# Kernel tuning notes

Measured on AMD Instinct MI355X. Metric: run time of the kernel, lower is better.

## Reference

```python
import jax, jax.numpy as jnp
import numpy as np

DIM = 64
HID = DIM // 8  # 8, hidden width of pos_fc / attn_fc
B, N, V = 1024, 64, 8
NUM_IDS = 10


def setup_inputs() -> dict:
    key = jax.random.key(0)
    ks = jax.random.split(key, 24)
    stdv = 1.0 / np.sqrt(DIM * DIM)
    inp = {
        "q": jax.random.normal(ks[0], (B, N, DIM), jnp.float32),
        "k": jax.random.normal(ks[1], (B, N, V, DIM), jnp.float32),
        "pos": jax.random.normal(ks[2], (B, N, V, 4), jnp.float32),
        "strength": jax.random.normal(ks[3], (512,), jnp.float32),
        # learned params
        "q_tbl": jax.random.uniform(ks[4], (NUM_IDS, DIM * DIM), jnp.float32, -stdv, stdv),
        "k_tbl": jax.random.uniform(ks[5], (NUM_IDS, DIM * DIM), jnp.float32, -stdv, stdv),
        "v_tbl": jax.random.uniform(ks[6], (NUM_IDS, DIM * DIM), jnp.float32, -stdv, stdv),
        "pos_w1": jax.random.normal(ks[7], (4, HID), jnp.float32) * 0.5,
        "pos_b1": jax.random.normal(ks[8], (HID,), jnp.float32) * 0.1,
        "pos_w2": jax.random.normal(ks[9], (HID, DIM), jnp.float32) * 0.2,
        "pos_b2": jax.random.normal(ks[10], (DIM,), jnp.float32) * 0.1,
        "attn_w1": jax.random.normal(ks[11], (DIM, HID), jnp.float32) * 0.1,
        "attn_b1": jax.random.normal(ks[12], (HID,), jnp.float32) * 0.1,
        "attn_w2": jax.random.normal(ks[13], (HID, DIM), jnp.float32) * 0.2,
        "attn_b2": jax.random.normal(ks[14], (DIM,), jnp.float32) * 0.1,
        "out_w": jax.random.normal(ks[15], (DIM, DIM), jnp.float32) * 0.1,
        "out_b": jax.random.normal(ks[16], (DIM,), jnp.float32) * 0.1,
        "str_w": jax.random.normal(ks[17], (512, DIM), jnp.float32) * 0.04,
        "str_b": jax.random.normal(ks[18], (DIM,), jnp.float32) * 0.1,
        # int args
        "mask": jax.random.randint(ks[19], (B, N, V, 1), 0, 2, jnp.int32),
        "embed_id1": 3,
    }
    return inp


def reference(q, k, pos, strength, q_tbl, k_tbl, v_tbl,
              pos_w1, pos_b1, pos_w2, pos_b2,
              attn_w1, attn_b1, attn_w2, attn_b2,
              out_w, out_b, str_w, str_b, mask, embed_id1):
    s = strength @ str_w + str_b                       # [DIM]
    Wq = q_tbl[embed_id1].reshape(DIM, DIM)
    Wk = k_tbl[embed_id1].reshape(DIM, DIM)
    Wv = v_tbl[embed_id1].reshape(DIM, DIM)
    # F.linear(x, W) = x @ W.T ; note v is computed from k (as in source)
    qh = q @ Wq.T + s                                  # [B,N,DIM]
    kh = k @ Wk.T + s                                  # [B,N,V,DIM]
    vh = k @ Wv.T + s                                  # [B,N,V,DIM]
    p = jax.nn.relu(pos @ pos_w1 + pos_b1) @ pos_w2 + pos_b2   # [B,N,V,DIM]
    attn = kh - qh[:, :, None, :] + p                  # [B,N,V,DIM]
    attn = jax.nn.relu(attn @ attn_w1 + attn_b1) @ attn_w2 + attn_b2
    attn = jnp.where(mask == 0, jnp.float32(-1e9), attn)
    attn = jax.nn.softmax(attn, axis=-2)               # softmax over views V
    x = ((vh + p) * attn).sum(axis=2)                  # [B,N,DIM]
    x = x @ out_w + out_b
    return x
```

## Files before the change

### kernel.cpp

```cpp
#include <hip/hip_runtime.h>

#define TBL 4096

#define WS_S    0
#define WS_AT   64
#define WS_BQT  (64 + 512)
#define WS_CT   (64 + 1024)
#define WS_C0   (64 + 1024 + 64)

typedef __attribute__((ext_vector_type(8))) short bf16x8;
typedef __attribute__((ext_vector_type(4))) float f32x4;

__device__ inline short f2bf(float f) {
    union { float f; unsigned u; } v; v.f = f;
    unsigned r = v.u + 0x7fffu + ((v.u >> 16) & 1u);
    return (short)(r >> 16);
}

__device__ inline bf16x8 pack8(const float* x) {
    bf16x8 r;
    #pragma unroll
    for (int i = 0; i < 8; ++i) r[i] = f2bf(x[i]);
    return r;
}

__device__ inline bf16x8 loadpack(const float* p) {
    float4 a = *(const float4*)p;
    float4 b = *(const float4*)(p + 4);
    float t[8] = {a.x, a.y, a.z, a.w, b.x, b.y, b.z, b.w};
    return pack8(t);
}

__device__ inline bf16x8 loadpackneg(const float* p) {
    float4 a = *(const float4*)p;
    float4 b = *(const float4*)(p + 4);
    float t[8] = {-a.x, -a.y, -a.z, -a.w, -b.x, -b.y, -b.z, -b.w};
    return pack8(t);
}

__global__ __launch_bounds__(256) void precompute_kernel(
    const float* __restrict__ strength, const float* __restrict__ str_w,
    const float* __restrict__ str_b,
    const float* __restrict__ q_tbl, const float* __restrict__ k_tbl,
    const float* __restrict__ attn_w1, const float* __restrict__ attn_b1,
    const float* __restrict__ pos_w2, const float* __restrict__ pos_b2,
    const int* __restrict__ embed_id, float* __restrict__ ws)
{
    __shared__ float red[4][64];
    const int t = threadIdx.x;
    const int blk = blockIdx.x;
    const int id = embed_id[0];
    if (blk == 0) {
        const int d = t & 63, part = t >> 6;
        float acc = 0.f;
        for (int i = part * 128; i < part * 128 + 128; ++i)
            acc += strength[i] * str_w[i * 64 + d];
        red[part][d] = acc;
        __syncthreads();
        if (t < 64)
            ws[WS_S + t] = red[0][t] + red[1][t] + red[2][t] + red[3][t] + str_b[t];
    } else if (blk <= 2) {
        const int h = (blk - 1) * 4 + (t >> 6);
        const int j = t & 63;
        const float* W = k_tbl + (size_t)id * TBL;
        float acc = 0.f;
        for (int d = 0; d < 64; ++d) acc += W[d * 64 + j] * attn_w1[d * 8 + h];
        ws[WS_AT + h * 64 + j] = acc;
    } else if (blk <= 4) {
        const int h = (blk - 3) * 4 + (t >> 6);
        const int j = t & 63;
        const float* W = q_tbl + (size_t)id * TBL;
        float acc = 0.f;
        for (int d = 0; d < 64; ++d) acc += W[d * 64 + j] * attn_w1[d * 8 + h];
        ws[WS_BQT + h * 64 + j] = acc;
    } else {
        if (t < 64) {
            const int h = t >> 3, g = t & 7;
            float acc = 0.f;
            for (int d = 0; d < 64; ++d) acc += pos_w2[g * 64 + d] * attn_w1[d * 8 + h];
            ws[WS_CT + t] = acc;
        } else if (t < 72) {
            const int h = t - 64;
            float acc = attn_b1[h];
            for (int d = 0; d < 64; ++d) acc += pos_b2[d] * attn_w1[d * 8 + h];
            ws[WS_C0 + h] = acc;
        }
    }
}

__global__ __launch_bounds__(256, 3) void attn2d_main(
    const float* __restrict__ q, const float* __restrict__ k,
    const float* __restrict__ pos, const float* __restrict__ v_tbl,
    const float* __restrict__ pos_w1, const float* __restrict__ pos_b1,
    const float* __restrict__ pos_w2, const float* __restrict__ pos_b2,
    const float* __restrict__ attn_w2, const float* __restrict__ attn_b2,
    const float* __restrict__ out_w, const float* __restrict__ out_b,
    const int* __restrict__ mask, const int* __restrict__ embed_id,
    const float* __restrict__ ws, float* __restrict__ out)
{
    __shared__ float vh_lds[4][16 * 68];
    __shared__ float x_lds[4][16 * 68];
    __shared__ float rhid_lds[4][16 * 12];
    __shared__ float hp_lds[4][16 * 8];

    const int tid  = threadIdx.x;
    const int lane = tid & 63;
    const int wiv  = __builtin_amdgcn_readfirstlane(tid >> 6);
    const int q4   = lane >> 4;
    const int col  = lane & 15;

    float* vh_w = vh_lds[wiv];
    float* x_w  = x_lds[wiv];
    float* rh_w = rhid_lds[wiv];
    float* hp_w = hp_lds[wiv];

    const int wid = blockIdx.x * 4 + wiv;
    const int id  = embed_id[0];

    bf16x8 Bv[4][2];
    #pragma unroll
    for (int t = 0; t < 4; ++t)
        #pragma unroll
        for (int c = 0; c < 2; ++c)
            Bv[t][c] = loadpack(v_tbl + (size_t)id * TBL +
                                (t * 16 + col) * 64 + c * 32 + q4 * 8);
    bf16x8 Bh[4];
    {
        bf16x8 z{};
        #pragma unroll
        for (int c = 0; c < 2; ++c)
            Bh[c] = (col < 8) ? loadpack(ws + WS_AT + col * 64 + c * 32 + q4 * 8) : z;
        #pragma unroll
        for (int c = 0; c < 2; ++c)
            Bh[2 + c] = (col < 8) ? loadpackneg(ws + WS_BQT + col * 64 + c * 32 + q4 * 8) : z;
    }
    bf16x8 Bct{};
    if (q4 == 0 && col < 8) Bct = loadpack(ws + WS_CT + col * 8);

    float w2ar[8], pw2r[8];
    #pragma unroll
    for (int h = 0; h < 8; ++h) w2ar[h] = attn_w2[h * 64 + lane];
    #pragma unroll
    for (int g = 0; g < 8; ++g) pw2r[g] = pos_w2[g * 64 + lane];
    const float sr   = ws[WS_S + lane];
    const float b2pr = pos_b2[lane];
    const float b2ar = attn_b2[lane];
    const float c0r  = (col < 8) ? ws[WS_C0 + col] : 0.f;

    #pragma unroll
    for (int it = 0; it < 4; ++it) {
        const int pair = wid * 4 + it;
        const int bn0  = pair * 2;

        bf16x8 Ak[2], Aq[2];
        #pragma unroll
        for (int c = 0; c < 2; ++c)
            Ak[c] = loadpack(k + ((size_t)pair * 16 + col) * 64 + c * 32 + q4 * 8);
        #pragma unroll
        for (int c = 0; c < 2; ++c)
            Aq[c] = loadpack(q + (size_t)(bn0 + (col >> 3)) * 64 + c * 32 + q4 * 8);

        bf16x8 Ahp{};
        if (lane < 16) {
            float4 pp = *(const float4*)(pos + ((size_t)pair * 16 + lane) * 4);
            float hv[8];
            #pragma unroll
            for (int g = 0; g < 8; ++g)
                hv[g] = fmaxf(pos_b1[g] + pp.x * pos_w1[g] + pp.y * pos_w1[8 + g] +
                              pp.z * pos_w1[16 + g] + pp.w * pos_w1[24 + g], 0.f);
            *(float4*)&hp_w[lane * 8]     = make_float4(hv[0], hv[1], hv[2], hv[3]);
            *(float4*)&hp_w[lane * 8 + 4] = make_float4(hv[4], hv[5], hv[6], hv[7]);
            Ahp = pack8(hv);
        }

        f32x4 acch = {0.f, 0.f, 0.f, 0.f};
        acch = __builtin_amdgcn_mfma_f32_16x16x32_bf16(Ak[0], Bh[0], acch, 0, 0, 0);
        acch = __builtin_amdgcn_mfma_f32_16x16x32_bf16(Ak[1], Bh[1], acch, 0, 0, 0);
        acch = __builtin_amdgcn_mfma_f32_16x16x32_bf16(Aq[0], Bh[2], acch, 0, 0, 0);
        acch = __builtin_amdgcn_mfma_f32_16x16x32_bf16(Aq[1], Bh[3], acch, 0, 0, 0);
        acch = __builtin_amdgcn_mfma_f32_16x16x32_bf16(Ahp,   Bct,   acch, 0, 0, 0);
        if (col < 8) {
            #pragma unroll
            for (int r = 0; r < 4; ++r)
                rh_w[(q4 * 4 + r) * 12 + col] = fmaxf(acch[r] + c0r, 0.f);
        }

        #pragma unroll
        for (int t = 0; t < 4; ++t) {
            f32x4 a = {0.f, 0.f, 0.f, 0.f};
            a = __builtin_amdgcn_mfma_f32_16x16x32_bf16(Ak[0], Bv[t][0], a, 0, 0, 0);
            a = __builtin_amdgcn_mfma_f32_16x16x32_bf16(Ak[1], Bv[t][1], a, 0, 0, 0);
            #pragma unroll
            for (int r = 0; r < 4; ++r)
                vh_w[(q4 * 4 + r) * 68 + t * 16 + col] = a[r];
        }

        #pragma unroll
        for (int bnp = 0; bnp < 2; ++bnp) {
            const int rb = bnp * 8;
            float att[8];
            #pragma unroll
            for (int v = 0; v < 8; ++v) {
                const float* rr = &rh_w[(rb + v) * 12];
                float4 r0 = *(const float4*)rr;
                float4 r1 = *(const float4*)(rr + 4);
                float a = b2ar
                        + r0.x * w2ar[0] + r0.y * w2ar[1] + r0.z * w2ar[2] + r0.w * w2ar[3]
                        + r1.x * w2ar[4] + r1.y * w2ar[5] + r1.z * w2ar[6] + r1.w * w2ar[7];
                att[v] = (mask[(size_t)(bn0 + bnp) * 8 + v] != 0) ? a : -1e9f;
            }
            float m = att[0];
            #pragma unroll
            for (int v = 1; v < 8; ++v) m = fmaxf(m, att[v]);
            float wgt[8], ssum = 0.f;
            #pragma unroll
            for (int v = 0; v < 8; ++v) { wgt[v] = __expf(att[v] - m); ssum += wgt[v]; }
            const float inv = __builtin_amdgcn_rcpf(ssum);
            float xacc = 0.f;
            #pragma unroll
            for (int v = 0; v < 8; ++v) {
                const float* hr = &hp_w[(rb + v) * 8];
                float4 h0 = *(const float4*)hr;
                float4 h1 = *(const float4*)(hr + 4);
                float pv = sr + b2pr
                         + h0.x * pw2r[0] + h0.y * pw2r[1] + h0.z * pw2r[2] + h0.w * pw2r[3]
                         + h1.x * pw2r[4] + h1.y * pw2r[5] + h1.z * pw2r[6] + h1.w * pw2r[7];
                xacc += (wgt[v] * inv) * (vh_w[(rb + v) * 68 + lane] + pv);
            }
            x_w[(it * 2 + bnp) * 68 + lane] = xacc;
        }
    }

    bf16x8 Ax[2];
    #pragma unroll
    for (int c = 0; c < 2; ++c)
        Ax[c] = loadpack(&x_w[col * 68 + c * 32 + q4 * 8]);
    #pragma unroll
    for (int t = 0; t < 4; ++t) {
        bf16x8 Bo0, Bo1;
        {
            float t0[8], t1[8];
            #pragma unroll
            for (int jj = 0; jj < 8; ++jj) {
                t0[jj] = out_w[(q4 * 8 + jj) * 64 + t * 16 + col];
                t1[jj] = out_w[(32 + q4 * 8 + jj) * 64 + t * 16 + col];
            }
            Bo0 = pack8(t0); Bo1 = pack8(t1);
        }
        f32x4 a = {0.f, 0.f, 0.f, 0.f};
        a = __builtin_amdgcn_mfma_f32_16x16x32_bf16(Ax[0], Bo0, a, 0, 0, 0);
        a = __builtin_amdgcn_mfma_f32_16x16x32_bf16(Ax[1], Bo1, a, 0, 0, 0);
        const float ob = out_b[t * 16 + col];
        #pragma unroll
        for (int r = 0; r < 4; ++r) {
            const int row = q4 * 4 + r;
            if (row < 8)
                out[((size_t)wid * 8 + row) * 64 + t * 16 + col] = a[r] + ob;
        }
    }
}

extern "C" void kernel_launch(void* const* d_in, const int* in_sizes, int n_in,
                              void* d_out, int out_size, void* d_ws, size_t ws_size,
                              hipStream_t stream) {
    const float* q        = (const float*)d_in[0];
    const float* k        = (const float*)d_in[1];
    const float* pos      = (const float*)d_in[2];
    const float* strength = (const float*)d_in[3];
    const float* q_tbl    = (const float*)d_in[4];
    const float* k_tbl    = (const float*)d_in[5];
    const float* v_tbl    = (const float*)d_in[6];
    const float* pos_w1   = (const float*)d_in[7];
    const float* pos_b1   = (const float*)d_in[8];
    const float* pos_w2   = (const float*)d_in[9];
    const float* pos_b2   = (const float*)d_in[10];
    const float* attn_w1  = (const float*)d_in[11];
    const float* attn_b1  = (const float*)d_in[12];
    const float* attn_w2  = (const float*)d_in[13];
    const float* attn_b2  = (const float*)d_in[14];
    const float* out_w    = (const float*)d_in[15];
    const float* out_b    = (const float*)d_in[16];
    const float* str_w    = (const float*)d_in[17];
    const float* str_b    = (const float*)d_in[18];
    const int*   mask     = (const int*)d_in[19];
    const int*   embed    = (const int*)d_in[20];
    float* ws  = (float*)d_ws;
    float* out = (float*)d_out;

    hipLaunchKernelGGL(precompute_kernel, dim3(6), dim3(256), 0, stream,
                       strength, str_w, str_b, q_tbl, k_tbl, attn_w1, attn_b1,
                       pos_w2, pos_b2, embed, ws);
    hipLaunchKernelGGL(attn2d_main, dim3(2048), dim3(256), 0, stream,
                       q, k, pos, v_tbl, pos_w1, pos_b1, pos_w2, pos_b2,
                       attn_w2, attn_b2, out_w, out_b, mask, embed, ws, out);
}
```

Measured before the change: 288.5 us.

## Move attention and position second layers onto MFMA with pre-packed bf16 weight images

The precompute kernel now writes every weight fragment the main kernel needs (Bh, Bct, v_tbl, pos_w2, attn_w2, out_w) into the workspace as pre-packed bf16 MFMA operands. Each wave then loads these fragments directly instead of converting from fp32 per block. The position MLP output and the attention second layer are computed with extra MFMAs fused into the vh accumulator. The per-view softmax uses the MFMA output layout with a ds_swizzle cross-lane reduction instead of LDS round trips, and bf16 packing uses v_cvt_pk_bf16_f32. This removes the vh and hp LDS buffers and scalar FMA loops and raises the occupancy hint, at the cost of rounding the hidden activations and pos_w2 to bf16.

After: 285.7 us. Within noise of the previous version (-1.0%).

```diff
diff --git a/kernel.cpp b/kernel.cpp
--- a/kernel.cpp
+++ b/kernel.cpp
@@ -2,26 +2,32 @@
 
 #define TBL 4096
 
-#define WS_S    0
-#define WS_AT   64
-#define WS_BQT  (64 + 512)
-#define WS_CT   (64 + 1024)
-#define WS_C0   (64 + 1024 + 64)
+#define WS_SPB 0
+#define WS_C0  64
+#define WS_IMG 128
+#define IMG_BH  0
+#define IMG_BCT 4
+#define IMG_BP  5
+#define IMG_BW2 9
+#define IMG_BV  13
+#define IMG_BO  21
 
 typedef __attribute__((ext_vector_type(8))) short bf16x8;
 typedef __attribute__((ext_vector_type(4))) float f32x4;
 
-__device__ inline short f2bf(float f) {
-    union { float f; unsigned u; } v; v.f = f;
-    unsigned r = v.u + 0x7fffu + ((v.u >> 16) & 1u);
-    return (short)(r >> 16);
+__device__ inline int cvt2bf(float a, float b) {
+    int r;
+    asm("v_cvt_pk_bf16_f32 %0, %1, %2" : "=v"(r) : "v"(a), "v"(b));
+    return r;
 }
 
 __device__ inline bf16x8 pack8(const float* x) {
-    bf16x8 r;
-    #pragma unroll
-    for (int i = 0; i < 8; ++i) r[i] = f2bf(x[i]);
-    return r;
+    union { int4 i; bf16x8 b; } u;
+    u.i.x = cvt2bf(x[0], x[1]);
+    u.i.y = cvt2bf(x[2], x[3]);
+    u.i.z = cvt2bf(x[4], x[5]);
+    u.i.w = cvt2bf(x[6], x[7]);
+    return u.b;
 }
 
 __device__ inline bf16x8 loadpack(const float* p) {
@@ -31,77 +37,99 @@
     return pack8(t);
 }
 
-__device__ inline bf16x8 loadpackneg(const float* p) {
-    float4 a = *(const float4*)p;
-    float4 b = *(const float4*)(p + 4);
-    float t[8] = {-a.x, -a.y, -a.z, -a.w, -b.x, -b.y, -b.z, -b.w};
-    return pack8(t);
-}
-
-__global__ __launch_bounds__(256) void precompute_kernel(
+__device__ inline float swz16(float x) {
+    return __int_as_float(__builtin_amdgcn_ds_swizzle(__float_as_int(x), 0x401F));
+}
+
+__global__ __launch_bounds__(64) void precompute_kernel(
     const float* __restrict__ strength, const float* __restrict__ str_w,
     const float* __restrict__ str_b,
     const float* __restrict__ q_tbl, const float* __restrict__ k_tbl,
+    const float* __restrict__ v_tbl, const float* __restrict__ out_w,
     const float* __restrict__ attn_w1, const float* __restrict__ attn_b1,
+    const float* __restrict__ attn_w2,
     const float* __restrict__ pos_w2, const float* __restrict__ pos_b2,
     const int* __restrict__ embed_id, float* __restrict__ ws)
 {
-    __shared__ float red[4][64];
-    const int t = threadIdx.x;
-    const int blk = blockIdx.x;
+    const int t  = threadIdx.x;
+    const int b  = blockIdx.x;
     const int id = embed_id[0];
-    if (blk == 0) {
-        const int d = t & 63, part = t >> 6;
+    const int q4 = t >> 4, col = t & 15;
+
+    if (b == 0) {
         float acc = 0.f;
-        for (int i = part * 128; i < part * 128 + 128; ++i)
-            acc += strength[i] * str_w[i * 64 + d];
-        red[part][d] = acc;
-        __syncthreads();
-        if (t < 64)
-            ws[WS_S + t] = red[0][t] + red[1][t] + red[2][t] + red[3][t] + str_b[t];
-    } else if (blk <= 2) {
-        const int h = (blk - 1) * 4 + (t >> 6);
-        const int j = t & 63;
-        const float* W = k_tbl + (size_t)id * TBL;
-        float acc = 0.f;
-        for (int d = 0; d < 64; ++d) acc += W[d * 64 + j] * attn_w1[d * 8 + h];
-        ws[WS_AT + h * 64 + j] = acc;
-    } else if (blk <= 4) {
-        const int h = (blk - 3) * 4 + (t >> 6);
-        const int j = t & 63;
-        const float* W = q_tbl + (size_t)id * TBL;
-        float acc = 0.f;
-        for (int d = 0; d < 64; ++d) acc += W[d * 64 + j] * attn_w1[d * 8 + h];
-        ws[WS_BQT + h * 64 + j] = acc;
+        for (int i = 0; i < 512; ++i) acc += strength[i] * str_w[i * 64 + t];
+        ws[WS_SPB + t] = acc + str_b[t] + pos_b2[t];
+        if (t < 8) {
+            float c = attn_b1[t];
+            for (int d = 0; d < 64; ++d) c += pos_b2[d] * attn_w1[d * 8 + t];
+            ws[WS_C0 + t] = c;
+        }
+        return;
+    }
+    const int im = b - 1;
+    float val[8];
+    #pragma unroll
+    for (int j = 0; j < 8; ++j) val[j] = 0.f;
+
+    if (im < 4) {
+        const int c = im;
+        const float* tbl = (c < 2 ? k_tbl : q_tbl) + (size_t)id * TBL;
+        const float sgn = (c < 2) ? 1.f : -1.f;
+        const int kb = (c & 1) * 32 + q4 * 8;
+        if (col < 8) {
+            for (int d = 0; d < 64; ++d) {
+                const float w = attn_w1[d * 8 + col];
+                #pragma unroll
+                for (int j = 0; j < 8; ++j) val[j] += tbl[d * 64 + kb + j] * w;
+            }
+            #pragma unroll
+            for (int j = 0; j < 8; ++j) val[j] *= sgn;
+        }
+    } else if (im == 4) {
+        if (q4 == 0 && col < 8) {
+            for (int d = 0; d < 64; ++d) {
+                const float w = attn_w1[d * 8 + col];
+                #pragma unroll
+                for (int j = 0; j < 8; ++j) val[j] += pos_w2[j * 64 + d] * w;
+            }
+        }
+    } else if (im < 9) {
+        const int tt = im - 5;
+        if (q4 == 0) {
+            #pragma unroll
+            for (int j = 0; j < 8; ++j) val[j] = pos_w2[j * 64 + tt * 16 + col];
+        }
+    } else if (im < 13) {
+        const int tt = im - 9;
+        if (q4 == 0) {
+            #pragma unroll
+            for (int j = 0; j < 8; ++j) val[j] = attn_w2[j * 64 + tt * 16 + col];
+        }
+    } else if (im < 21) {
+        const int e = im - 13, tt = e >> 1, c = e & 1;
+        #pragma unroll
+        for (int j = 0; j < 8; ++j)
+            val[j] = v_tbl[(size_t)id * TBL + (tt * 16 + col) * 64 + c * 32 + q4 * 8 + j];
     } else {
-        if (t < 64) {
-            const int h = t >> 3, g = t & 7;
-            float acc = 0.f;
-            for (int d = 0; d < 64; ++d) acc += pos_w2[g * 64 + d] * attn_w1[d * 8 + h];
-            ws[WS_CT + t] = acc;
-        } else if (t < 72) {
-            const int h = t - 64;
-            float acc = attn_b1[h];
-            for (int d = 0; d < 64; ++d) acc += pos_b2[d] * attn_w1[d * 8 + h];
-            ws[WS_C0 + h] = acc;
-        }
-    }
-}
-
-__global__ __launch_bounds__(256, 3) void attn2d_main(
+        const int e = im - 21, tt = e >> 1, c = e & 1;
+        #pragma unroll
+        for (int j = 0; j < 8; ++j)
+            val[j] = out_w[(c * 32 + q4 * 8 + j) * 64 + tt * 16 + col];
+    }
+    ((bf16x8*)(ws + WS_IMG))[im * 64 + t] = pack8(val);
+}
+
+__global__ __launch_bounds__(256, 4) void attn2d_main(
     const float* __restrict__ q, const float* __restrict__ k,
-    const float* __restrict__ pos, const float* __restrict__ v_tbl,
+    const float* __restrict__ pos,
     const float* __restrict__ pos_w1, const float* __restrict__ pos_b1,
-    const float* __restrict__ pos_w2, const float* __restrict__ pos_b2,
-    const float* __restrict__ attn_w2, const float* __restrict__ attn_b2,
-    const float* __restrict__ out_w, const float* __restrict__ out_b,
-    const int* __restrict__ mask, const int* __restrict__ embed_id,
+    const float* __restrict__ attn_b2, const float* __restrict__ out_b,
+    const int* __restrict__ mask,
     const float* __restrict__ ws, float* __restrict__ out)
 {
-    __shared__ float vh_lds[4][16 * 68];
-    __shared__ float x_lds[4][16 * 68];
-    __shared__ float rhid_lds[4][16 * 12];
-    __shared__ float hp_lds[4][16 * 8];
+    __shared__ float rh_lds[4][16 * 12];
+    __shared__ float x_lds[4][8 * 68];
 
     const int tid  = threadIdx.x;
     const int lane = tid & 63;
@@ -109,43 +137,25 @@
     const int q4   = lane >> 4;
     const int col  = lane & 15;
 
-    float* vh_w = vh_lds[wiv];
+    float* rh_w = rh_lds[wiv];
     float* x_w  = x_lds[wiv];
-    float* rh_w = rhid_lds[wiv];
-    float* hp_w = hp_lds[wiv];
 
     const int wid = blockIdx.x * 4 + wiv;
-    const int id  = embed_id[0];
-
-    bf16x8 Bv[4][2];
-    #pragma unroll
-    for (int t = 0; t < 4; ++t)
-        #pragma unroll
-        for (int c = 0; c < 2; ++c)
-            Bv[t][c] = loadpack(v_tbl + (size_t)id * TBL +
-                                (t * 16 + col) * 64 + c * 32 + q4 * 8);
+    const bf16x8* img = (const bf16x8*)(ws + WS_IMG);
+
     bf16x8 Bh[4];
-    {
-        bf16x8 z{};
-        #pragma unroll
-        for (int c = 0; c < 2; ++c)
-            Bh[c] = (col < 8) ? loadpack(ws + WS_AT + col * 64 + c * 32 + q4 * 8) : z;
-        #pragma unroll
-        for (int c = 0; c < 2; ++c)
-            Bh[2 + c] = (col < 8) ? loadpackneg(ws + WS_BQT + col * 64 + c * 32 + q4 * 8) : z;
-    }
-    bf16x8 Bct{};
-    if (q4 == 0 && col < 8) Bct = loadpack(ws + WS_CT + col * 8);
-
-    float w2ar[8], pw2r[8];
-    #pragma unroll
-    for (int h = 0; h < 8; ++h) w2ar[h] = attn_w2[h * 64 + lane];
-    #pragma unroll
-    for (int g = 0; g < 8; ++g) pw2r[g] = pos_w2[g * 64 + lane];
-    const float sr   = ws[WS_S + lane];
-    const float b2pr = pos_b2[lane];
-    const float b2ar = attn_b2[lane];
-    const float c0r  = (col < 8) ? ws[WS_C0 + col] : 0.f;
+    #pragma unroll
+    for (int c = 0; c < 4; ++c) Bh[c] = img[(IMG_BH + c) * 64 + lane];
+    const bf16x8 Bct = img[IMG_BCT * 64 + lane];
+
+    float spb[4], b2a[4];
+    #pragma unroll
+    for (int t = 0; t < 4; ++t) {
+        spb[t] = ws[WS_SPB + t * 16 + col];
+        b2a[t] = attn_b2[t * 16 + col];
+    }
+    const float c0r = (col < 8) ? ws[WS_C0 + col] : 0.f;
+    const int bnp = q4 >> 1;
 
     #pragma unroll
     for (int it = 0; it < 4; ++it) {
@@ -159,6 +169,9 @@
         #pragma unroll
         for (int c = 0; c < 2; ++c)
             Aq[c] = loadpack(q + (size_t)(bn0 + (col >> 3)) * 64 + c * 32 + q4 * 8);
+
+        const int4 m4v = *(const int4*)(mask + (size_t)pair * 16 + q4 * 4);
+        const int mm[4] = {m4v.x, m4v.y, m4v.z, m4v.w};
 
         bf16x8 Ahp{};
         if (lane < 16) {
@@ -168,8 +181,6 @@
             for (int g = 0; g < 8; ++g)
                 hv[g] = fmaxf(pos_b1[g] + pp.x * pos_w1[g] + pp.y * pos_w1[8 + g] +
                               pp.z * pos_w1[16 + g] + pp.w * pos_w1[24 + g], 0.f);
-            *(float4*)&hp_w[lane * 8]     = make_float4(hv[0], hv[1], hv[2], hv[3]);
-            *(float4*)&hp_w[lane * 8 + 4] = make_float4(hv[4], hv[5], hv[6], hv[7]);
             Ahp = pack8(hv);
         }
 
@@ -185,68 +196,58 @@
                 rh_w[(q4 * 4 + r) * 12 + col] = fmaxf(acch[r] + c0r, 0.f);
         }
 
+        bf16x8 Arh{};
+        if (q4 == 0) {
+            float4 a  = *(const float4*)&rh_w[col * 12];
+            float4 bb = *(const float4*)&rh_w[col * 12 + 4];
+            float rr[8] = {a.x, a.y, a.z, a.w, bb.x, bb.y, bb.z, bb.w};
+            Arh = pack8(rr);
+        }
+
         #pragma unroll
         for (int t = 0; t < 4; ++t) {
-            f32x4 a = {0.f, 0.f, 0.f, 0.f};
-            a = __builtin_amdgcn_mfma_f32_16x16x32_bf16(Ak[0], Bv[t][0], a, 0, 0, 0);
-            a = __builtin_amdgcn_mfma_f32_16x16x32_bf16(Ak[1], Bv[t][1], a, 0, 0, 0);
+            const bf16x8 Bv0 = img[(IMG_BV + t * 2) * 64 + lane];
+            const bf16x8 Bv1 = img[(IMG_BV + t * 2 + 1) * 64 + lane];
+            const bf16x8 Bp  = img[(IMG_BP + t) * 64 + lane];
+            const bf16x8 Bw  = img[(IMG_BW2 + t) * 64 + lane];
+
+            f32x4 vh = {0.f, 0.f, 0.f, 0.f};
+            vh = __builtin_amdgcn_mfma_f32_16x16x32_bf16(Ak[0], Bv0, vh, 0, 0, 0);
+            vh = __builtin_amdgcn_mfma_f32_16x16x32_bf16(Ak[1], Bv1, vh, 0, 0, 0);
+            vh = __builtin_amdgcn_mfma_f32_16x16x32_bf16(Ahp,   Bp,  vh, 0, 0, 0);
+            f32x4 at = {0.f, 0.f, 0.f, 0.f};
+            at = __builtin_amdgcn_mfma_f32_16x16x32_bf16(Arh, Bw, at, 0, 0, 0);
+
+            float lg[4];
             #pragma unroll
             for (int r = 0; r < 4; ++r)
-                vh_w[(q4 * 4 + r) * 68 + t * 16 + col] = a[r];
-        }
-
-        #pragma unroll
-        for (int bnp = 0; bnp < 2; ++bnp) {
-            const int rb = bnp * 8;
-            float att[8];
-            #pragma unroll
-            for (int v = 0; v < 8; ++v) {
-                const float* rr = &rh_w[(rb + v) * 12];
-                float4 r0 = *(const float4*)rr;
-                float4 r1 = *(const float4*)(rr + 4);
-                float a = b2ar
-                        + r0.x * w2ar[0] + r0.y * w2ar[1] + r0.z * w2ar[2] + r0.w * w2ar[3]
-                        + r1.x * w2ar[4] + r1.y * w2ar[5] + r1.z * w2ar[6] + r1.w * w2ar[7];
-                att[v] = (mask[(size_t)(bn0 + bnp) * 8 + v] != 0) ? a : -1e9f;
+                lg[r] = (mm[r] != 0) ? (at[r] + b2a[t]) : -1e9f;
+
+            float mx = fmaxf(fmaxf(lg[0], lg[1]), fmaxf(lg[2], lg[3]));
+            mx = fmaxf(mx, swz16(mx));
+            float wsum = 0.f, xp = 0.f;
+            #pragma unroll
+            for (int r = 0; r < 4; ++r) {
+                const float wv = __expf(lg[r] - mx);
+                wsum += wv;
+                xp   += wv * (vh[r] + spb[t]);
             }
-            float m = att[0];
-            #pragma unroll
-            for (int v = 1; v < 8; ++v) m = fmaxf(m, att[v]);
-            float wgt[8], ssum = 0.f;
-            #pragma unroll
-            for (int v = 0; v < 8; ++v) { wgt[v] = __expf(att[v] - m); ssum += wgt[v]; }
-            const float inv = __builtin_amdgcn_rcpf(ssum);
-            float xacc = 0.f;
-            #pragma unroll
-            for (int v = 0; v < 8; ++v) {
-                const float* hr = &hp_w[(rb + v) * 8];
-                float4 h0 = *(const float4*)hr;
-                float4 h1 = *(const float4*)(hr + 4);
-                float pv = sr + b2pr
-                         + h0.x * pw2r[0] + h0.y * pw2r[1] + h0.z * pw2r[2] + h0.w * pw2r[3]
-                         + h1.x * pw2r[4] + h1.y * pw2r[5] + h1.z * pw2r[6] + h1.w * pw2r[7];
-                xacc += (wgt[v] * inv) * (vh_w[(rb + v) * 68 + lane] + pv);
-            }
-            x_w[(it * 2 + bnp) * 68 + lane] = xacc;
+            wsum += swz16(wsum);
+            xp   += swz16(xp);
+            const float xv = xp * __builtin_amdgcn_rcpf(wsum);
+            if ((q4 & 1) == 0)
+                x_w[(it * 2 + bnp) * 68 + t * 16 + col] = xv;
         }
     }
 
     bf16x8 Ax[2];
     #pragma unroll
     for (int c = 0; c < 2; ++c)
-        Ax[c] = loadpack(&x_w[col * 68 + c * 32 + q4 * 8]);
+        Ax[c] = loadpack(&x_w[(col & 7) * 68 + c * 32 + q4 * 8]);
     #pragma unroll
     for (int t = 0; t < 4; ++t) {
-        bf16x8 Bo0, Bo1;
-        {
-            float t0[8], t1[8];
-            #pragma unroll
-            for (int jj = 0; jj < 8; ++jj) {
-                t0[jj] = out_w[(q4 * 8 + jj) * 64 + t * 16 + col];
-                t1[jj] = out_w[(32 + q4 * 8 + jj) * 64 + t * 16 + col];
-            }
-            Bo0 = pack8(t0); Bo1 = pack8(t1);
-        }
+        const bf16x8 Bo0 = img[(IMG_BO + t * 2) * 64 + lane];
+        const bf16x8 Bo1 = img[(IMG_BO + t * 2 + 1) * 64 + lane];
         f32x4 a = {0.f, 0.f, 0.f, 0.f};
         a = __builtin_amdgcn_mfma_f32_16x16x32_bf16(Ax[0], Bo0, a, 0, 0, 0);
         a = __builtin_amdgcn_mfma_f32_16x16x32_bf16(Ax[1], Bo1, a, 0, 0, 0);
@@ -287,10 +288,9 @@
     float* ws  = (float*)d_ws;
     float* out = (float*)d_out;
 
-    hipLaunchKernelGGL(precompute_kernel, dim3(6), dim3(256), 0, stream,
-                       strength, str_w, str_b, q_tbl, k_tbl, attn_w1, attn_b1,
-                       pos_w2, pos_b2, embed, ws);
+    hipLaunchKernelGGL(precompute_kernel, dim3(30), dim3(64), 0, stream,
+                       strength, str_w, str_b, q_tbl, k_tbl, v_tbl, out_w,
+                       attn_w1, attn_b1, attn_w2, pos_w2, pos_b2, embed, ws);
     hipLaunchKernelGGL(attn2d_main, dim3(2048), dim3(256), 0, stream,
-                       q, k, pos, v_tbl, pos_w1, pos_b1, pos_w2, pos_b2,
-                       attn_w2, attn_b2, out_w, out_b, mask, embed, ws, out);
-}
+                       q, k, pos, pos_w1, pos_b1, attn_b2, out_b, mask, ws, out);
+}
```
